# Performance work log

Hardware: AMD Instinct MI355X
Metric: run time of the kernel (lower is better)

The kernel has to match this reference:

```python
import jax, jax.numpy as jnp
import numpy as np

N_NODES = 100000
N_EDGES = 1600000
IN_FEATS = 128
NUM_HEADS = 4
OUT_FEATS = 32
NUM_ETYPES = 8
DROP_BLOCKS = 4


def setup_inputs() -> dict:
    key = jax.random.key(0)
    k1, k2, k3, k4, k5 = jax.random.split(key, 5)
    feat = jax.random.normal(k1, (N_NODES, IN_FEATS), dtype=jnp.float32)
    e_feat = jax.random.randint(k2, (N_EDGES,), 0, NUM_ETYPES, dtype=jnp.int32)
    src = jax.random.randint(k3, (N_EDGES,), 0, N_NODES, dtype=jnp.int32)
    dst = jax.random.randint(k4, (N_EDGES,), 0, N_NODES, dtype=jnp.int32)
    kf, ke = jax.random.split(k5)
    # xavier_normal with relu gain for fc: std = gain * sqrt(2/(fan_in+fan_out))
    gain = float(np.sqrt(2.0))
    std = gain * float(np.sqrt(2.0 / (IN_FEATS + NUM_HEADS * OUT_FEATS)))
    fc_weight = jax.random.normal(kf, (NUM_HEADS * OUT_FEATS, IN_FEATS), dtype=jnp.float32) * std
    # edge_emb initialized with normal_()
    edge_emb = jax.random.normal(ke, (NUM_ETYPES, NUM_HEADS), dtype=jnp.float32)
    return {"feat": feat, "fc_weight": fc_weight, "edge_emb": edge_emb,
            "e_feat": e_feat, "src": src, "dst": dst, "drop_blocks": DROP_BLOCKS}


def _edge_softmax(e, dst, n_nodes):
    # segmented softmax over incoming edges per destination node, per head
    # e: (E, H)
    m = jax.ops.segment_max(e, dst, num_segments=n_nodes)      # (N, H)
    z = jnp.exp(e - m[dst])                                    # (E, H)
    s = jax.ops.segment_sum(z, dst, num_segments=n_nodes)      # (N, H)
    return z / s[dst]


def reference(feat, fc_weight, edge_emb, e_feat, src, dst, drop_blocks):
    n = feat.shape[0]
    H = edge_emb.shape[1]
    D = fc_weight.shape[0] // H
    # fc projection -> (N, H, D); feat_drop is identity (p=0 / eval)
    ft = (feat @ fc_weight.T).reshape(n, H, D)
    # edge type embedding logits (E, H)
    ee = edge_emb[e_feat]
    attn = _edge_softmax(ee, dst, n)                           # (E, H)
    # mcdropedge with attn_drop p=0: attn broadcast over blocks is identity scaling
    # u_mul_e + sum: gather src features, scale by attn, scatter-sum into dst
    msg = ft[src] * attn[:, :, None]                           # (E, H, D)
    rst = jax.ops.segment_sum(msg, dst, num_segments=n)        # (N, H, D)
    # attn returned with mcdropedge expansion shape (E, H, drop_blocks, 1)
    attn_out = jnp.broadcast_to(attn[:, :, None], (attn.shape[0], H, drop_blocks))[..., None]
    return rst, attn_out
```

## Files before the change

### kernel.cpp

```cpp
#include <hip/hip_runtime.h>


typedef short short8 __attribute__((ext_vector_type(8)));
typedef unsigned short ushort8 __attribute__((ext_vector_type(8)));
typedef float f32x4 __attribute__((ext_vector_type(4)));

__device__ inline unsigned short f2bf(float x) {
    unsigned u = __builtin_bit_cast(unsigned, x);
    u += 0x7FFFu + ((u >> 16) & 1u);
    return (unsigned short)(u >> 16);
}

__device__ inline short8 cvt8(float4 lo, float4 hi) {
    short8 t;
    t[0] = (short)f2bf(lo.x); t[1] = (short)f2bf(lo.y);
    t[2] = (short)f2bf(lo.z); t[3] = (short)f2bf(lo.w);
    t[4] = (short)f2bf(hi.x); t[5] = (short)f2bf(hi.y);
    t[6] = (short)f2bf(hi.z); t[7] = (short)f2bf(hi.w);
    return t;
}

__device__ inline void nt_store4(float* p, float a, float b, float c, float d) {
    f32x4 v = (f32x4){a, b, c, d};
    __builtin_nontemporal_store(v, (f32x4*)p);
}

__global__ __launch_bounds__(256) void k_bcnt(const int* __restrict__ dst,
                                              unsigned* __restrict__ gpart, int E,
                                              const float* __restrict__ W,
                                              unsigned short* __restrict__ Wb) {
    __shared__ unsigned l[256];
    int tid = threadIdx.x;
    if (blockIdx.x < 8) {
        int i = blockIdx.x * 2048 + tid * 8;
        float4 lo = *(const float4*)(W + i);
        float4 hi = *(const float4*)(W + i + 4);
        *(ushort8*)(Wb + i) = __builtin_bit_cast(ushort8, cvt8(lo, hi));
    }
    l[tid] = 0;
    __syncthreads();
    int base = blockIdx.x * 4096;
#pragma unroll
    for (int j = 0; j < 16; ++j) {
        int e = base + j * 256 + tid;
        if (e < E) atomicAdd(&l[(unsigned)dst[e] >> 9], 1u);
    }
    __syncthreads();
    gpart[blockIdx.x * 256 + tid] = l[tid];
}

__global__ __launch_bounds__(256) void k_bscan(const unsigned* __restrict__ gpart,
                                               int nchunk,
                                               unsigned* __restrict__ gbase,
                                               unsigned* __restrict__ gcur) {
    __shared__ unsigned s[256];
    int t = threadIdx.x;
    unsigned sum = 0;
    int r = 0;
    for (; r + 4 <= nchunk; r += 4) {
        unsigned a0 = gpart[(r + 0) * 256 + t];
        unsigned a1 = gpart[(r + 1) * 256 + t];
        unsigned a2 = gpart[(r + 2) * 256 + t];
        unsigned a3 = gpart[(r + 3) * 256 + t];
        sum += a0 + a1 + a2 + a3;
    }
    for (; r < nchunk; ++r) sum += gpart[r * 256 + t];
    unsigned orig = sum;
    s[t] = sum;
    __syncthreads();
    for (int of = 1; of < 256; of <<= 1) {
        unsigned v = (t >= of) ? s[t - of] : 0u;
        __syncthreads();
        s[t] += v;
        __syncthreads();
    }
    unsigned eb = s[t] - orig;
    gbase[t] = eb;
    gcur[t] = eb;
}

__global__ __launch_bounds__(256) void k_partgemm(
        const int* __restrict__ src, const int* __restrict__ dst,
        const int* __restrict__ ef, unsigned* __restrict__ gcur,
        unsigned* __restrict__ csr2, int E, int nbuk, int gemmBlocks,
        const float* __restrict__ feat, const unsigned short* __restrict__ Wb,
        unsigned short* __restrict__ ftb, int N) {
    __shared__ unsigned short Sb[128 * 136];
    int tid = threadIdx.x;
    int bid = blockIdx.x;

    if (bid >= gemmBlocks) {
        unsigned* lcnt = (unsigned*)Sb;
        unsigned* lbase = lcnt + 256;
        unsigned* lcur = lbase + 256;
        unsigned* gw2 = lcur + 256;
        unsigned* stp = gw2 + 256;
        unsigned short* stb = (unsigned short*)(stp + 4096);
        int rid = bid - gemmBlocks;
        lcnt[tid] = 0;
        __syncthreads();

        int cb = rid * 4096;
        int cc = E - cb; if (cc > 4096) cc = 4096;

        unsigned pay[16];
        unsigned short bk[16];
#pragma unroll
        for (int j = 0; j < 16; ++j) {
            int idx = j * 256 + tid;
            if (idx < cc) {
                int e = cb + idx;
                unsigned d = (unsigned)dst[e];
                pay[j] = (unsigned)src[e] | ((unsigned)ef[e] << 17) | ((d & 511u) << 20);
                bk[j] = (unsigned short)(d >> 9);
                atomicAdd(&lcnt[bk[j]], 1u);
            }
        }
        __syncthreads();
        lbase[tid] = lcnt[tid];
        __syncthreads();
        for (int of = 1; of < 256; of <<= 1) {
            unsigned v = (tid >= of) ? lbase[tid - of] : 0u;
            __syncthreads();
            lbase[tid] += v;
            __syncthreads();
        }
        unsigned eb = lbase[tid] - lcnt[tid];
        __syncthreads();
        lbase[tid] = eb;
        lcur[tid] = eb;
        __syncthreads();
#pragma unroll
        for (int j = 0; j < 16; ++j) {
            int idx = j * 256 + tid;
            if (idx < cc) {
                unsigned lpos = atomicAdd(&lcur[bk[j]], 1u);
                stp[lpos] = pay[j];
                stb[lpos] = bk[j];
            }
        }
        if (tid < nbuk && lcnt[tid]) gw2[tid] = atomicAdd(&gcur[tid], lcnt[tid]);
        __syncthreads();
#pragma unroll
        for (int j = 0; j < 16; ++j) {
            int i = j * 256 + tid;
            if (i < cc) {
                unsigned b = stb[i];
                csr2[gw2[b] + (i - lbase[b])] = stp[i];
            }
        }
        return;
    }

    int row0 = bid * 64;

#pragma unroll
    for (int it = 0; it < 8; ++it) {
        int idx = it * 2048 + tid * 8;
        int r = idx >> 7, c = idx & 127;
        ushort8 v = *(const ushort8*)(Wb + idx);
        *(ushort8*)((char*)Sb + (((unsigned)(r * 256 + c * 2)) ^ (unsigned)((r & 7) << 4))) = v;
    }

    int wv = tid >> 6, lane = tid & 63;
    int rl = lane & 15;
    unsigned swz = (unsigned)((lane & 7) << 4);
    int kq = (lane >> 4) * 16;
    int ko = (lane >> 4) * 8;

    int ra = row0 + wv * 16 + rl;
    int rc = ra < N - 1 ? ra : N - 1;
    const float* ap = feat + (size_t)rc * 128 + ko;

    float4 f[8];
#pragma unroll
    for (int kk = 0; kk < 4; ++kk) {
        f[2 * kk]     = *(const float4*)(ap + kk * 32);
        f[2 * kk + 1] = *(const float4*)(ap + kk * 32 + 4);
    }
    __syncthreads();

    f32x4 acc[8];
#pragma unroll
    for (int jt = 0; jt < 8; ++jt) acc[jt] = (f32x4){0.f, 0.f, 0.f, 0.f};

    const char* Bb = (const char*)Sb;
#pragma unroll
    for (int kk = 0; kk < 4; ++kk) {
        short8 a = cvt8(f[2 * kk], f[2 * kk + 1]);
        int kb = kk * 64 + kq;
#pragma unroll
        for (int jt = 0; jt < 8; ++jt) {
            short8 bj = *(const short8*)(Bb + (((unsigned)((jt * 16 + rl) * 256 + kb)) ^ swz));
            acc[jt] = __builtin_amdgcn_mfma_f32_16x16x32_bf16(a, bj, acc[jt], 0, 0, 0);
        }
    }

    __syncthreads();
#pragma unroll
    for (int jt = 0; jt < 8; ++jt) {
        int col = jt * 16 + rl;
        int rbase = wv * 16 + ((lane >> 4) << 2);
#pragma unroll
        for (int rg = 0; rg < 4; ++rg)
            Sb[(rbase + rg) * 136 + col] = f2bf(acc[jt][rg]);
    }
    __syncthreads();
#pragma unroll
    for (int g = 0; g < 4; ++g) {
        int rloc = g * 16 + (tid >> 4);
        int cc = (tid & 15) * 8;
        int gr = row0 + rloc;
        if (gr < N) {
            ushort8 v = *(const ushort8*)(&Sb[rloc * 136 + cc]);
            *(ushort8*)(ftb + (size_t)gr * 128 + cc) = v;
        }
    }
}

__global__ __launch_bounds__(256) void k_bsort2(const unsigned* __restrict__ csr2,
                                                const unsigned* __restrict__ gbase,
                                                const unsigned* __restrict__ gend,
                                                const float* __restrict__ emb,
                                                unsigned* __restrict__ csr,
                                                unsigned* __restrict__ offs,
                                                unsigned* __restrict__ deg,
                                                float* __restrict__ stats, int N) {
    __shared__ unsigned cnt8[512 * 8];
    __shared__ unsigned degL[512];
    __shared__ unsigned offsL[512];
    __shared__ unsigned curL[512];
    __shared__ unsigned tmp[256];
    __shared__ float se[32];
    int b = blockIdx.x, tid = threadIdx.x;
    if (tid < 32) se[tid] = emb[tid];
#pragma unroll
    for (int i = 0; i < 16; ++i) cnt8[i * 256 + tid] = 0u;
    __syncthreads();
    unsigned r0 = gbase[b], r1 = gend[b];
    for (unsigned i = r0 + tid; i < r1; i += 256) {
        unsigned en = csr2[i];
        atomicAdd(&cnt8[((en >> 20) & 511u) * 8u + ((en >> 17) & 7u)], 1u);
    }
    __syncthreads();
    int n0 = tid * 2, n1 = tid * 2 + 1;
    unsigned d0 = 0, d1 = 0;
#pragma unroll
    for (int k = 0; k < 8; ++k) { d0 += cnt8[n0 * 8 + k]; d1 += cnt8[n1 * 8 + k]; }
    degL[n0] = d0; degL[n1] = d1;
    tmp[tid] = d0 + d1;
    __syncthreads();
    for (int of = 1; of < 256; of <<= 1) {
        unsigned v = (tid >= of) ? tmp[tid - of] : 0u;
        __syncthreads();
        tmp[tid] += v;
        __syncthreads();
    }
    unsigned eb = tmp[tid] - (d0 + d1);
    offsL[n0] = eb;        curL[n0] = eb;
    offsL[n1] = eb + d0;   curL[n1] = eb + d0;
#pragma unroll
    for (int q = 0; q < 2; ++q) {
        int nl = tid * 2 + q;
        int gn = b * 512 + nl;
        if (gn < N) {
            offs[gn] = r0 + offsL[nl];
            unsigned dg = degL[nl];
            deg[gn] = dg;
            const unsigned* c = &cnt8[nl * 8];
#pragma unroll
            for (int h = 0; h < 4; ++h) {
                float m = -3.4e38f;
#pragma unroll
                for (int tt = 0; tt < 8; ++tt)
                    if (c[tt]) m = fmaxf(m, se[tt * 4 + h]);
                float s = 0.f;
#pragma unroll
                for (int tt = 0; tt < 8; ++tt)
                    if (c[tt]) s += (float)c[tt] * expf(se[tt * 4 + h] - m);
                stats[(size_t)gn * 8 + h] = m;
                stats[(size_t)gn * 8 + 4 + h] = dg ? (1.0f / s) : 0.0f;
            }
        }
    }
    __syncthreads();
    for (unsigned i = r0 + tid; i < r1; i += 256) {
        unsigned en = csr2[i];
        unsigned nlo = (en >> 20) & 511u;
        unsigned tt = (en >> 17) & 7u;
        unsigned pos = r0 + atomicAdd(&curL[nlo], 1u);
        csr[pos] = (en & 0x1FFFFu) | (tt << 20);
    }
}

__global__ __launch_bounds__(256) void k_aggattn(
        const unsigned* __restrict__ csr, const unsigned* __restrict__ offs,
        const unsigned* __restrict__ deg, const float* __restrict__ stats,
        const float* __restrict__ emb, const uint4* __restrict__ ft4,
        float* __restrict__ rst, int N, int aggBlocks,
        const int* __restrict__ e_feat, const int* __restrict__ dst,
        float* __restrict__ ao, int E) {
    __shared__ float sbuf[4 * 257];
    int tid = threadIdx.x;
    int bid = blockIdx.x;

    if (bid >= aggBlocks) {
        int rid = bid - aggBlocks;
        size_t lim = (size_t)E * 4;
#pragma unroll 1
        for (int r4 = 0; r4 < 4; ++r4) {
            int e = (rid * 4 + r4) * 256 + tid;
            float a0 = 0.f, a1 = 0.f, a2 = 0.f, a3 = 0.f;
            if (e < E) {
                int tt = e_feat[e];
                int d = dst[e];
                const float4* st4 = (const float4*)(stats + (size_t)d * 8);
                float4 m4 = st4[0], i4 = st4[1];
                float4 ee = *(const float4*)(emb + tt * 4);
                a0 = expf(ee.x - m4.x) * i4.x;
                a1 = expf(ee.y - m4.y) * i4.y;
                a2 = expf(ee.z - m4.z) * i4.z;
                a3 = expf(ee.w - m4.w) * i4.w;
            }
            __syncthreads();
            sbuf[0 * 257 + tid] = a0;
            sbuf[1 * 257 + tid] = a1;
            sbuf[2 * 257 + tid] = a2;
            sbuf[3 * 257 + tid] = a3;
            __syncthreads();
            size_t base = (size_t)(rid * 4 + r4) * 1024;
#pragma unroll
            for (int r = 0; r < 4; ++r) {
                size_t g = base + r * 256 + tid;
                if (g < lim) {
                    int gl = r * 256 + tid;
                    float v = sbuf[(gl & 3) * 257 + (gl >> 2)];
                    nt_store4(ao + g * 4, v, v, v, v);
                }
            }
        }
        return;
    }

    float* wl = sbuf;
    int wv = tid >> 6, lane = tid & 63;
    int nbase = (bid * 4 + wv) * 2;
    {
        int nn = lane >> 5;
        int idx = lane & 31;
        int n = nbase + nn;
        if (n < N) {
            int tt = idx >> 2, hh = idx & 3;
            float m = stats[(size_t)n * 8 + hh];
            float is = stats[(size_t)n * 8 + 4 + hh];
            wl[wv * 64 + lane] = expf(emb[tt * 4 + hh] - m) * is;
        }
    }
    __syncthreads();
    int cl = lane & 15;
    int es = lane >> 4;
    int h = cl >> 2;

#pragma unroll 1
    for (int nn = 0; nn < 2; ++nn) {
        int n = __builtin_amdgcn_readfirstlane(nbase + nn);
        if (n >= N) break;
        unsigned o = offs[n], dg = deg[n];
        const float* wlh = wl + wv * 64 + nn * 32 + h;
        float acc[8];
#pragma unroll
        for (int i = 0; i < 8; ++i) acc[i] = 0.f;

        for (unsigned kb = 0; kb < dg; kb += 64) {
            unsigned rem = dg - kb; if (rem > 64) rem = 64;
            unsigned centry = 0;
            if (lane < (int)rem) centry = csr[o + kb + lane];
            unsigned g = 0;
            for (; g + 16 <= rem; g += 16) {
                uint4 f[4]; float a[4];
#pragma unroll
                for (int q = 0; q < 4; ++q) {
                    unsigned e = __shfl(centry, (int)(g + q * 4 + es), 64);
                    f[q] = ft4[(size_t)(e & 0xFFFFFu) * 16 + cl];
                    a[q] = wlh[(e >> 20) * 4];
                }
#pragma unroll
                for (int q = 0; q < 4; ++q) {
                    acc[0] = fmaf(a[q], __builtin_bit_cast(float, f[q].x << 16), acc[0]);
                    acc[1] = fmaf(a[q], __builtin_bit_cast(float, f[q].x & 0xFFFF0000u), acc[1]);
                    acc[2] = fmaf(a[q], __builtin_bit_cast(float, f[q].y << 16), acc[2]);
                    acc[3] = fmaf(a[q], __builtin_bit_cast(float, f[q].y & 0xFFFF0000u), acc[3]);
                    acc[4] = fmaf(a[q], __builtin_bit_cast(float, f[q].z << 16), acc[4]);
                    acc[5] = fmaf(a[q], __builtin_bit_cast(float, f[q].z & 0xFFFF0000u), acc[5]);
                    acc[6] = fmaf(a[q], __builtin_bit_cast(float, f[q].w << 16), acc[6]);
                    acc[7] = fmaf(a[q], __builtin_bit_cast(float, f[q].w & 0xFFFF0000u), acc[7]);
                }
            }
            for (; g < rem; g += 4) {
                int eidx = (int)g + es;
                bool valid = eidx < (int)rem;
                unsigned e = __shfl(centry, valid ? eidx : (int)g, 64);
                uint4 f = ft4[(size_t)(e & 0xFFFFFu) * 16 + cl];
                float a = valid ? wlh[(e >> 20) * 4] : 0.f;
                acc[0] = fmaf(a, __builtin_bit_cast(float, f.x << 16), acc[0]);
                acc[1] = fmaf(a, __builtin_bit_cast(float, f.x & 0xFFFF0000u), acc[1]);
                acc[2] = fmaf(a, __builtin_bit_cast(float, f.y << 16), acc[2]);
                acc[3] = fmaf(a, __builtin_bit_cast(float, f.y & 0xFFFF0000u), acc[3]);
                acc[4] = fmaf(a, __builtin_bit_cast(float, f.z << 16), acc[4]);
                acc[5] = fmaf(a, __builtin_bit_cast(float, f.z & 0xFFFF0000u), acc[5]);
                acc[6] = fmaf(a, __builtin_bit_cast(float, f.w << 16), acc[6]);
                acc[7] = fmaf(a, __builtin_bit_cast(float, f.w & 0xFFFF0000u), acc[7]);
            }
        }
#pragma unroll
        for (int i = 0; i < 8; ++i) {
            acc[i] += __shfl_xor(acc[i], 16, 64);
            acc[i] += __shfl_xor(acc[i], 32, 64);
        }
        if (lane < 16) {
            float* op = rst + (size_t)n * 128 + cl * 8;
            nt_store4(op, acc[0], acc[1], acc[2], acc[3]);
            nt_store4(op + 4, acc[4], acc[5], acc[6], acc[7]);
        }
    }
}

extern "C" void kernel_launch(void* const* d_in, const int* in_sizes, int n_in,
                              void* d_out, int out_size, void* d_ws, size_t ws_size,
                              hipStream_t stream) {
    const float* feat = (const float*)d_in[0];
    const float* W = (const float*)d_in[1];
    const float* emb = (const float*)d_in[2];
    const int* e_feat = (const int*)d_in[3];
    const int* src = (const int*)d_in[4];
    const int* dst = (const int*)d_in[5];
    int N = in_sizes[0] / 128;
    int E = in_sizes[3];
    int nbuk = (N + 511) >> 9;
    int nchunk = (E + 4095) / 4096;
    int gemmBlocks = (N + 63) / 64;
    int aggBlocks = (N + 7) / 8;
    int attnBlocks = (E + 1023) / 1024;

    char* ws = (char*)d_ws;
    size_t off = 0;
    auto alloc = [&](size_t bytes) {
        void* p = ws + off;
        off = (off + bytes + 255) & ~(size_t)255;
        return p;
    };
    unsigned short* ftb = (unsigned short*)alloc((size_t)N * 128 * 2);
    unsigned short* Wb = (unsigned short*)alloc((size_t)in_sizes[1] * 2);
    float* stats = (float*)alloc((size_t)N * 8 * 4);
    unsigned* deg = (unsigned*)alloc((size_t)N * 4);
    unsigned* offs = (unsigned*)alloc((size_t)N * 4);
    unsigned* csr = (unsigned*)alloc((size_t)E * 4);
    unsigned* csr2 = (unsigned*)alloc((size_t)E * 4);
    unsigned* gpart = (unsigned*)alloc((size_t)nchunk * 256 * 4);
    unsigned* gbase = (unsigned*)alloc(256 * 4);
    unsigned* gcur = (unsigned*)alloc(256 * 4);

    float* rst = (float*)d_out;
    float* ao = (float*)d_out + (size_t)N * 128;

    k_bcnt<<<nchunk, 256, 0, stream>>>(dst, gpart, E, W, Wb);
    k_bscan<<<1, 256, 0, stream>>>(gpart, nchunk, gbase, gcur);
    k_partgemm<<<gemmBlocks + nchunk, 256, 0, stream>>>(
        src, dst, e_feat, gcur, csr2, E, nbuk, gemmBlocks, feat, Wb, ftb, N);
    k_bsort2<<<nbuk, 256, 0, stream>>>(csr2, gbase, gcur, emb, csr, offs, deg, stats, N);
    k_aggattn<<<aggBlocks + attnBlocks, 256, 0, stream>>>(
        csr, offs, deg, stats, emb, (const uint4*)ftb, rst, N, aggBlocks,
        e_feat, dst, ao, E);
}
```

Measured before the change: 167.1 us.

## Slice feature layout per 16-column group, split GEMM across sort kernels, atomic bucket counts

Stores the projected bf16 features in eight column-slice planes so each aggregation block gathers only 32 bytes per edge for one slice, and remaps aggregation to blocks of 32 nodes per slice with pair lanes over edges. Half of the GEMM tiles move into the bucket-sort kernel so the sort stage overlaps with projection work. Bucket counts are accumulated with global atomics after a memset, replacing the partial-count array and its reduction in the scan. The aim is better cache locality on the gather and less idle time in the small sort grid, at the cost of more aggregation blocks and extra shuffle reductions.

New measurement: 439.4 us. 163% more time.

```diff
diff --git a/kernel.cpp b/kernel.cpp
--- a/kernel.cpp
+++ b/kernel.cpp
@@ -26,7 +26,7 @@
 }
 
 __global__ __launch_bounds__(256) void k_bcnt(const int* __restrict__ dst,
-                                              unsigned* __restrict__ gpart, int E,
+                                              unsigned* __restrict__ gcnt, int E,
                                               const float* __restrict__ W,
                                               unsigned short* __restrict__ Wb) {
     __shared__ unsigned l[256];
@@ -46,27 +46,16 @@
         if (e < E) atomicAdd(&l[(unsigned)dst[e] >> 9], 1u);
     }
     __syncthreads();
-    gpart[blockIdx.x * 256 + tid] = l[tid];
-}
-
-__global__ __launch_bounds__(256) void k_bscan(const unsigned* __restrict__ gpart,
-                                               int nchunk,
+    if (l[tid]) atomicAdd(&gcnt[tid], l[tid]);
+}
+
+__global__ __launch_bounds__(256) void k_bscan(const unsigned* __restrict__ gcnt,
                                                unsigned* __restrict__ gbase,
                                                unsigned* __restrict__ gcur) {
     __shared__ unsigned s[256];
     int t = threadIdx.x;
-    unsigned sum = 0;
-    int r = 0;
-    for (; r + 4 <= nchunk; r += 4) {
-        unsigned a0 = gpart[(r + 0) * 256 + t];
-        unsigned a1 = gpart[(r + 1) * 256 + t];
-        unsigned a2 = gpart[(r + 2) * 256 + t];
-        unsigned a3 = gpart[(r + 3) * 256 + t];
-        sum += a0 + a1 + a2 + a3;
-    }
-    for (; r < nchunk; ++r) sum += gpart[r * 256 + t];
-    unsigned orig = sum;
-    s[t] = sum;
+    unsigned orig = gcnt[t];
+    s[t] = orig;
     __syncthreads();
     for (int of = 1; of < 256; of <<= 1) {
         unsigned v = (t >= of) ? s[t - of] : 0u;
@@ -79,81 +68,10 @@
     gcur[t] = eb;
 }
 
-__global__ __launch_bounds__(256) void k_partgemm(
-        const int* __restrict__ src, const int* __restrict__ dst,
-        const int* __restrict__ ef, unsigned* __restrict__ gcur,
-        unsigned* __restrict__ csr2, int E, int nbuk, int gemmBlocks,
-        const float* __restrict__ feat, const unsigned short* __restrict__ Wb,
-        unsigned short* __restrict__ ftb, int N) {
-    __shared__ unsigned short Sb[128 * 136];
-    int tid = threadIdx.x;
-    int bid = blockIdx.x;
-
-    if (bid >= gemmBlocks) {
-        unsigned* lcnt = (unsigned*)Sb;
-        unsigned* lbase = lcnt + 256;
-        unsigned* lcur = lbase + 256;
-        unsigned* gw2 = lcur + 256;
-        unsigned* stp = gw2 + 256;
-        unsigned short* stb = (unsigned short*)(stp + 4096);
-        int rid = bid - gemmBlocks;
-        lcnt[tid] = 0;
-        __syncthreads();
-
-        int cb = rid * 4096;
-        int cc = E - cb; if (cc > 4096) cc = 4096;
-
-        unsigned pay[16];
-        unsigned short bk[16];
-#pragma unroll
-        for (int j = 0; j < 16; ++j) {
-            int idx = j * 256 + tid;
-            if (idx < cc) {
-                int e = cb + idx;
-                unsigned d = (unsigned)dst[e];
-                pay[j] = (unsigned)src[e] | ((unsigned)ef[e] << 17) | ((d & 511u) << 20);
-                bk[j] = (unsigned short)(d >> 9);
-                atomicAdd(&lcnt[bk[j]], 1u);
-            }
-        }
-        __syncthreads();
-        lbase[tid] = lcnt[tid];
-        __syncthreads();
-        for (int of = 1; of < 256; of <<= 1) {
-            unsigned v = (tid >= of) ? lbase[tid - of] : 0u;
-            __syncthreads();
-            lbase[tid] += v;
-            __syncthreads();
-        }
-        unsigned eb = lbase[tid] - lcnt[tid];
-        __syncthreads();
-        lbase[tid] = eb;
-        lcur[tid] = eb;
-        __syncthreads();
-#pragma unroll
-        for (int j = 0; j < 16; ++j) {
-            int idx = j * 256 + tid;
-            if (idx < cc) {
-                unsigned lpos = atomicAdd(&lcur[bk[j]], 1u);
-                stp[lpos] = pay[j];
-                stb[lpos] = bk[j];
-            }
-        }
-        if (tid < nbuk && lcnt[tid]) gw2[tid] = atomicAdd(&gcur[tid], lcnt[tid]);
-        __syncthreads();
-#pragma unroll
-        for (int j = 0; j < 16; ++j) {
-            int i = j * 256 + tid;
-            if (i < cc) {
-                unsigned b = stb[i];
-                csr2[gw2[b] + (i - lbase[b])] = stp[i];
-            }
-        }
-        return;
-    }
-
-    int row0 = bid * 64;
-
+__device__ __forceinline__ void gemm_tile(int row0, const float* __restrict__ feat,
+                                          const unsigned short* __restrict__ Wb,
+                                          unsigned short* __restrict__ ftb, int N,
+                                          unsigned short* Sb, int tid) {
 #pragma unroll
     for (int it = 0; it < 8; ++it) {
         int idx = it * 2048 + tid * 8;
@@ -206,6 +124,8 @@
             Sb[(rbase + rg) * 136 + col] = f2bf(acc[jt][rg]);
     }
     __syncthreads();
+    int s = (tid & 15) >> 1;
+    int hf = tid & 1;
 #pragma unroll
     for (int g = 0; g < 4; ++g) {
         int rloc = g * 16 + (tid >> 4);
@@ -213,26 +133,109 @@
         int gr = row0 + rloc;
         if (gr < N) {
             ushort8 v = *(const ushort8*)(&Sb[rloc * 136 + cc]);
-            *(ushort8*)(ftb + (size_t)gr * 128 + cc) = v;
-        }
-    }
-}
-
-__global__ __launch_bounds__(256) void k_bsort2(const unsigned* __restrict__ csr2,
-                                                const unsigned* __restrict__ gbase,
-                                                const unsigned* __restrict__ gend,
-                                                const float* __restrict__ emb,
-                                                unsigned* __restrict__ csr,
-                                                unsigned* __restrict__ offs,
-                                                unsigned* __restrict__ deg,
-                                                float* __restrict__ stats, int N) {
-    __shared__ unsigned cnt8[512 * 8];
-    __shared__ unsigned degL[512];
-    __shared__ unsigned offsL[512];
-    __shared__ unsigned curL[512];
-    __shared__ unsigned tmp[256];
-    __shared__ float se[32];
-    int b = blockIdx.x, tid = threadIdx.x;
+            *(ushort8*)(ftb + (size_t)s * N * 16 + (size_t)gr * 16 + hf * 8) = v;
+        }
+    }
+}
+
+__global__ __launch_bounds__(256) void k_gempart(
+        const int* __restrict__ src, const int* __restrict__ dst,
+        const int* __restrict__ ef, unsigned* __restrict__ gcur,
+        unsigned* __restrict__ csr2, int E, int nbuk, int gemmABlocks,
+        const float* __restrict__ feat, const unsigned short* __restrict__ Wb,
+        unsigned short* __restrict__ ftb, int N) {
+    __shared__ unsigned short Sb[128 * 136];
+    int tid = threadIdx.x;
+    int bid = blockIdx.x;
+
+    if (bid < gemmABlocks) {
+        gemm_tile(bid * 64, feat, Wb, ftb, N, Sb, tid);
+        return;
+    }
+    unsigned* lcnt = (unsigned*)Sb;
+    unsigned* lbase = lcnt + 256;
+    unsigned* lcur = lbase + 256;
+    unsigned* gw2 = lcur + 256;
+    unsigned* stp = gw2 + 256;
+    unsigned short* stb = (unsigned short*)(stp + 4096);
+    int rid = bid - gemmABlocks;
+    lcnt[tid] = 0;
+    __syncthreads();
+
+    int cb = rid * 4096;
+    int cc = E - cb; if (cc > 4096) cc = 4096;
+
+    unsigned pay[16];
+    unsigned short bk[16];
+#pragma unroll
+    for (int j = 0; j < 16; ++j) {
+        int idx = j * 256 + tid;
+        if (idx < cc) {
+            int e = cb + idx;
+            unsigned d = (unsigned)dst[e];
+            pay[j] = (unsigned)src[e] | ((unsigned)ef[e] << 17) | ((d & 511u) << 20);
+            bk[j] = (unsigned short)(d >> 9);
+            atomicAdd(&lcnt[bk[j]], 1u);
+        }
+    }
+    __syncthreads();
+    lbase[tid] = lcnt[tid];
+    __syncthreads();
+    for (int of = 1; of < 256; of <<= 1) {
+        unsigned v = (tid >= of) ? lbase[tid - of] : 0u;
+        __syncthreads();
+        lbase[tid] += v;
+        __syncthreads();
+    }
+    unsigned eb = lbase[tid] - lcnt[tid];
+    __syncthreads();
+    lbase[tid] = eb;
+    lcur[tid] = eb;
+    __syncthreads();
+#pragma unroll
+    for (int j = 0; j < 16; ++j) {
+        int idx = j * 256 + tid;
+        if (idx < cc) {
+            unsigned lpos = atomicAdd(&lcur[bk[j]], 1u);
+            stp[lpos] = pay[j];
+            stb[lpos] = bk[j];
+        }
+    }
+    if (tid < nbuk && lcnt[tid]) gw2[tid] = atomicAdd(&gcur[tid], lcnt[tid]);
+    __syncthreads();
+#pragma unroll
+    for (int j = 0; j < 16; ++j) {
+        int i = j * 256 + tid;
+        if (i < cc) {
+            unsigned b = stb[i];
+            csr2[gw2[b] + (i - lbase[b])] = stp[i];
+        }
+    }
+}
+
+__global__ __launch_bounds__(256) void k_sortgemm(
+        const unsigned* __restrict__ csr2, const unsigned* __restrict__ gbase,
+        const unsigned* __restrict__ gend, const float* __restrict__ emb,
+        unsigned* __restrict__ csr, unsigned* __restrict__ offs,
+        unsigned* __restrict__ deg, float* __restrict__ stats, int N, int nbuk,
+        int gemmRowTileOff,
+        const float* __restrict__ feat, const unsigned short* __restrict__ Wb,
+        unsigned short* __restrict__ ftb) {
+    __shared__ unsigned short Sb[128 * 136];
+    int tid = threadIdx.x;
+    int bid = blockIdx.x;
+
+    if (bid >= nbuk) {
+        gemm_tile((gemmRowTileOff + bid - nbuk) * 64, feat, Wb, ftb, N, Sb, tid);
+        return;
+    }
+    unsigned* cnt8 = (unsigned*)Sb;
+    unsigned* degL = cnt8 + 4096;
+    unsigned* offsL = degL + 512;
+    unsigned* curL = offsL + 512;
+    unsigned* tmp = curL + 512;
+    float* se = (float*)(tmp + 256);
+    int b = bid;
     if (tid < 32) se[tid] = emb[tid];
 #pragma unroll
     for (int i = 0; i < 16; ++i) cnt8[i * 256 + tid] = 0u;
@@ -344,29 +347,30 @@
 
     float* wl = sbuf;
     int wv = tid >> 6, lane = tid & 63;
-    int nbase = (bid * 4 + wv) * 2;
+    int s = bid & 7;
+    int h = s >> 1;
+    int nbase = (bid >> 3) * 32 + wv * 8;
     {
-        int nn = lane >> 5;
-        int idx = lane & 31;
+        int nn = lane >> 3, tt = lane & 7;
         int n = nbase + nn;
+        float v = 0.f;
         if (n < N) {
-            int tt = idx >> 2, hh = idx & 3;
-            float m = stats[(size_t)n * 8 + hh];
-            float is = stats[(size_t)n * 8 + 4 + hh];
-            wl[wv * 64 + lane] = expf(emb[tt * 4 + hh] - m) * is;
-        }
-    }
-    __syncthreads();
-    int cl = lane & 15;
-    int es = lane >> 4;
-    int h = cl >> 2;
+            float m = stats[(size_t)n * 8 + h];
+            float is = stats[(size_t)n * 8 + 4 + h];
+            v = expf(emb[tt * 4 + h] - m) * is;
+        }
+        wl[wv * 64 + lane] = v;
+    }
+    int pr = lane >> 1;
+    int hf = lane & 1;
+    size_t sliceBase = (size_t)s * N * 2;
 
 #pragma unroll 1
-    for (int nn = 0; nn < 2; ++nn) {
-        int n = __builtin_amdgcn_readfirstlane(nbase + nn);
+    for (int q = 0; q < 8; ++q) {
+        int n = __builtin_amdgcn_readfirstlane(nbase + q);
         if (n >= N) break;
         unsigned o = offs[n], dg = deg[n];
-        const float* wlh = wl + wv * 64 + nn * 32 + h;
+        const float* wln = wl + wv * 64 + q * 8;
         float acc[8];
 #pragma unroll
         for (int i = 0; i < 8; ++i) acc[i] = 0.f;
@@ -374,34 +378,14 @@
         for (unsigned kb = 0; kb < dg; kb += 64) {
             unsigned rem = dg - kb; if (rem > 64) rem = 64;
             unsigned centry = 0;
-            if (lane < (int)rem) centry = csr[o + kb + lane];
-            unsigned g = 0;
-            for (; g + 16 <= rem; g += 16) {
-                uint4 f[4]; float a[4];
-#pragma unroll
-                for (int q = 0; q < 4; ++q) {
-                    unsigned e = __shfl(centry, (int)(g + q * 4 + es), 64);
-                    f[q] = ft4[(size_t)(e & 0xFFFFFu) * 16 + cl];
-                    a[q] = wlh[(e >> 20) * 4];
-                }
-#pragma unroll
-                for (int q = 0; q < 4; ++q) {
-                    acc[0] = fmaf(a[q], __builtin_bit_cast(float, f[q].x << 16), acc[0]);
-                    acc[1] = fmaf(a[q], __builtin_bit_cast(float, f[q].x & 0xFFFF0000u), acc[1]);
-                    acc[2] = fmaf(a[q], __builtin_bit_cast(float, f[q].y << 16), acc[2]);
-                    acc[3] = fmaf(a[q], __builtin_bit_cast(float, f[q].y & 0xFFFF0000u), acc[3]);
-                    acc[4] = fmaf(a[q], __builtin_bit_cast(float, f[q].z << 16), acc[4]);
-                    acc[5] = fmaf(a[q], __builtin_bit_cast(float, f[q].z & 0xFFFF0000u), acc[5]);
-                    acc[6] = fmaf(a[q], __builtin_bit_cast(float, f[q].w << 16), acc[6]);
-                    acc[7] = fmaf(a[q], __builtin_bit_cast(float, f[q].w & 0xFFFF0000u), acc[7]);
-                }
-            }
-            for (; g < rem; g += 4) {
-                int eidx = (int)g + es;
-                bool valid = eidx < (int)rem;
-                unsigned e = __shfl(centry, valid ? eidx : (int)g, 64);
-                uint4 f = ft4[(size_t)(e & 0xFFFFFu) * 16 + cl];
-                float a = valid ? wlh[(e >> 20) * 4] : 0.f;
+            if (lane < (int)rem) centry = __builtin_nontemporal_load(csr + o + kb + lane);
+#pragma unroll 2
+            for (unsigned g = 0; g < rem; g += 32) {
+                int ei = (int)g + pr;
+                bool valid = ei < (int)rem;
+                unsigned e = __shfl(centry, valid ? ei : 0, 64);
+                uint4 f = ft4[sliceBase + (size_t)(e & 0xFFFFFu) * 2 + hf];
+                float a = valid ? wln[e >> 20] : 0.f;
                 acc[0] = fmaf(a, __builtin_bit_cast(float, f.x << 16), acc[0]);
                 acc[1] = fmaf(a, __builtin_bit_cast(float, f.x & 0xFFFF0000u), acc[1]);
                 acc[2] = fmaf(a, __builtin_bit_cast(float, f.y << 16), acc[2]);
@@ -414,11 +398,14 @@
         }
 #pragma unroll
         for (int i = 0; i < 8; ++i) {
+            acc[i] += __shfl_xor(acc[i], 2, 64);
+            acc[i] += __shfl_xor(acc[i], 4, 64);
+            acc[i] += __shfl_xor(acc[i], 8, 64);
             acc[i] += __shfl_xor(acc[i], 16, 64);
             acc[i] += __shfl_xor(acc[i], 32, 64);
         }
-        if (lane < 16) {
-            float* op = rst + (size_t)n * 128 + cl * 8;
+        if (lane < 2) {
+            float* op = rst + (size_t)n * 128 + s * 16 + hf * 8;
             nt_store4(op, acc[0], acc[1], acc[2], acc[3]);
             nt_store4(op + 4, acc[4], acc[5], acc[6], acc[7]);
         }
@@ -438,8 +425,10 @@
     int E = in_sizes[3];
     int nbuk = (N + 511) >> 9;
     int nchunk = (E + 4095) / 4096;
-    int gemmBlocks = (N + 63) / 64;
-    int aggBlocks = (N + 7) / 8;
+    int gemmTiles = (N + 63) / 64;
+    int gemmA = gemmTiles / 2;
+    int gemmB = gemmTiles - gemmA;
+    int aggBlocks = ((N + 31) / 32) * 8;
     int attnBlocks = (E + 1023) / 1024;
 
     char* ws = (char*)d_ws;
@@ -456,18 +445,20 @@
     unsigned* offs = (unsigned*)alloc((size_t)N * 4);
     unsigned* csr = (unsigned*)alloc((size_t)E * 4);
     unsigned* csr2 = (unsigned*)alloc((size_t)E * 4);
-    unsigned* gpart = (unsigned*)alloc((size_t)nchunk * 256 * 4);
+    unsigned* gcnt = (unsigned*)alloc(256 * 4);
     unsigned* gbase = (unsigned*)alloc(256 * 4);
     unsigned* gcur = (unsigned*)alloc(256 * 4);
 
     float* rst = (float*)d_out;
     float* ao = (float*)d_out + (size_t)N * 128;
 
-    k_bcnt<<<nchunk, 256, 0, stream>>>(dst, gpart, E, W, Wb);
-    k_bscan<<<1, 256, 0, stream>>>(gpart, nchunk, gbase, gcur);
-    k_partgemm<<<gemmBlocks + nchunk, 256, 0, stream>>>(
-        src, dst, e_feat, gcur, csr2, E, nbuk, gemmBlocks, feat, Wb, ftb, N);
-    k_bsort2<<<nbuk, 256, 0, stream>>>(csr2, gbase, gcur, emb, csr, offs, deg, stats, N);
+    hipMemsetAsync(gcnt, 0, 256 * 4, stream);
+    k_bcnt<<<nchunk, 256, 0, stream>>>(dst, gcnt, E, W, Wb);
+    k_bscan<<<1, 256, 0, stream>>>(gcnt, gbase, gcur);
+    k_gempart<<<gemmA + nchunk, 256, 0, stream>>>(
+        src, dst, e_feat, gcur, csr2, E, nbuk, gemmA, feat, Wb, ftb, N);
+    k_sortgemm<<<nbuk + gemmB, 256, 0, stream>>>(
+        csr2, gbase, gcur, emb, csr, offs, deg, stats, N, nbuk, gemmA, feat, Wb, ftb);
     k_aggattn<<<aggBlocks + attnBlocks, 256, 0, stream>>>(
         csr, offs, deg, stats, emb, (const uint4*)ftb, rst, N, aggBlocks,
         e_feat, dst, ao, E);
```
